# Performance work log

Measured on AMD Instinct MI355X. Metric: run time of the kernel, lower is better.

Reference implementation:

```python
import jax, jax.numpy as jnp
import numpy as np

EPS = 1e-5


def _conv3x3(x, w):
    # x: [B,C,H,W], w: [O,I,3,3], stride 1, padding 1
    return jax.lax.conv_general_dilated(
        x, w, window_strides=(1, 1), padding=((1, 1), (1, 1)),
        dimension_numbers=("NCHW", "OIHW", "NCHW"))


def _bn(x, g, b, m, v):
    # inference-mode BatchNorm2d over channel dim
    inv = jax.lax.rsqrt(v + EPS) * g
    return x * inv[None, :, None, None] + (b - m * inv)[None, :, None, None]


def setup_inputs() -> dict:
    key = jax.random.key(0)
    B, C, H, W = 32, 256, 56, 56
    ks = jax.random.split(key, 16)
    x = jax.random.normal(ks[0], (B, C, H, W), dtype=jnp.float32)
    mask = (jax.random.uniform(ks[1], (B, 1, H, W)) < 0.5).astype(jnp.float32)
    # dilated mask = 3x3 max-pool of mask
    mask_dilate = jax.lax.reduce_window(
        mask, -jnp.inf, jax.lax.max, (1, 1, 3, 3), (1, 1, 1, 1), "SAME")
    mask_dilate = jnp.maximum(mask_dilate, 0.0).astype(jnp.float32)
    vector = (jax.random.uniform(ks[2], (B, C)) < 0.5).astype(jnp.float32)
    conv1_w = jax.random.normal(ks[3], (C, C, 3, 3), dtype=jnp.float32) * 0.05
    conv2_w = jax.random.normal(ks[4], (C, C, 3, 3), dtype=jnp.float32) * 0.05
    bn1_g = 1.0 + 0.1 * jax.random.normal(ks[5], (C,), dtype=jnp.float32)
    bn1_b = 0.1 * jax.random.normal(ks[6], (C,), dtype=jnp.float32)
    bn1_m = 0.1 * jax.random.normal(ks[7], (C,), dtype=jnp.float32)
    bn1_v = 0.5 + jax.random.uniform(ks[8], (C,), dtype=jnp.float32)
    bn2_g = 1.0 + 0.1 * jax.random.normal(ks[9], (C,), dtype=jnp.float32)
    bn2_b = 0.1 * jax.random.normal(ks[10], (C,), dtype=jnp.float32)
    bn2_m = 0.1 * jax.random.normal(ks[11], (C,), dtype=jnp.float32)
    bn2_v = 0.5 + jax.random.uniform(ks[12], (C,), dtype=jnp.float32)
    return dict(x=x, mask=mask, mask_dilate=mask_dilate, vector=vector,
                conv1_w=conv1_w, bn1_g=bn1_g, bn1_b=bn1_b, bn1_m=bn1_m, bn1_v=bn1_v,
                conv2_w=conv2_w, bn2_g=bn2_g, bn2_b=bn2_b, bn2_m=bn2_m, bn2_v=bn2_v)


def reference(x, mask, mask_dilate, vector,
              conv1_w, bn1_g, bn1_b, bn1_m, bn1_v,
              conv2_w, bn2_g, bn2_b, bn2_m, bn2_v):
    # Sparse BasicBlock, stride=1, no downsample, input_mask=True.
    identity = x
    h = x * mask_dilate                      # apply_mask(x, mask_dilate)
    h = _conv3x3(h, conv1_w) * mask          # conv3x3_mask(conv1, ...)
    h = jax.nn.relu(_bn(h, bn1_g, bn1_b, bn1_m, bn1_v)) * mask_dilate  # bn_relu_mask(bn1, relu, ., mask_dilate)
    h = h * mask                             # apply_mask(x, mask)
    h = h * vector[:, :, None, None]         # channel_process(x, vector)
    h = _conv3x3(h, conv2_w) * mask          # conv3x3_mask(conv2, ...)
    h = _bn(h, bn2_g, bn2_b, bn2_m, bn2_v) * mask  # bn_relu_mask(bn2, None, ., mask)
    out = identity + h * mask                # identity + apply_mask(x, mask)
    return jax.nn.relu(out)
```

## Files before the change

kernel.cpp:

```cpp
#include <hip/hip_runtime.h>
#include <cstdint>


#define EPS 1e-5f

constexpr int Bn = 32, Cc = 256, Hh = 56, Ww = 56;
constexpr int HW = Hh * Ww;
constexpr int WP_ELEMS = 2 * 16 * 9 * 2 * 128 * 8;

typedef __bf16 bf16x8 __attribute__((ext_vector_type(8)));
typedef float  f32x16 __attribute__((ext_vector_type(16)));

__global__ void pack_xm(const float* __restrict__ x, const float* __restrict__ md,
                        __bf16* __restrict__ xm) {
    int blk = blockIdx.x, tid = threadIdx.x;
    int p = tid & 31, cg = tid >> 5;
    int px0 = blk * 32;
    int img = blk / 98;
    int s = (blk - img * 98) * 32 + p;
    float mdv = md[px0 + p];
    #pragma unroll
    for (int it = 0; it < 4; ++it) {
        int c = cg * 8 + it * 64;
        bf16x8 v;
        #pragma unroll
        for (int j = 0; j < 8; ++j)
            v[j] = (__bf16)(x[(size_t)(img * Cc + c + j) * HW + s] * mdv);
        *(bf16x8*)&xm[(size_t)(px0 + p) * Cc + c] = v;
    }
}

__global__ void pack_w(const float* __restrict__ w1, const float* __restrict__ w2,
                       __bf16* __restrict__ wp1, __bf16* __restrict__ wp2) {
    int id = blockIdx.x * 256 + threadIdx.x;
    const float* w = blockIdx.y ? w2 : w1;
    __bf16* wp = blockIdx.y ? wp2 : wp1;
    int j = id & 7; int t = id >> 3;
    int col = t & 127; t >>= 7;
    int half = t & 1; t >>= 1;
    int tap = t % 9; t /= 9;
    int chunk = t & 15; int coblk = t >> 4;
    int co = coblk * 128 + col;
    int ci = chunk * 16 + half * 8 + j;
    wp[id] = (__bf16)(w[((size_t)co * Cc + ci) * 9 + tap]);
}

__global__ void bn_prep(const float* g1, const float* b1, const float* m1, const float* v1,
                        const float* g2, const float* b2, const float* m2, const float* v2,
                        float* binv1, float* bbeta1, float* binv2, float* bbeta2) {
    int c = threadIdx.x;
    float i1 = g1[c] * rsqrtf(v1[c] + EPS);
    binv1[c] = i1; bbeta1[c] = b1[c] - m1[c] * i1;
    float i2 = g2[c] * rsqrtf(v2[c] + EPS);
    binv2[c] = i2; bbeta2[c] = b2[c] - m2[c] * i2;
}

__device__ __forceinline__ void gl_lds16(const __bf16* g, __bf16* l) {
    __builtin_amdgcn_global_load_lds(
        (const __attribute__((address_space(1))) void*)g,
        (__attribute__((address_space(3))) void*)l, 16, 0, 0);
}

template <bool C1>
__global__ __launch_bounds__(256, 2)
void conv_kern(const __bf16* __restrict__ src,
               const __bf16* __restrict__ wp,
               const float* __restrict__ maskg,
               const float* __restrict__ vec,
               const float* __restrict__ binv, const float* __restrict__ bbeta,
               const float* __restrict__ xin,
               void* __restrict__ dstv) {
    __shared__ __align__(16) __bf16 s_in[2 * 6 * 66 * 8];
    __shared__ __align__(16) __bf16 s_w[9 * 2 * 128 * 8];

    const int tid = threadIdx.x;
    const int lane = tid & 63, wave = tid >> 6;
    const int xlane = lane & 31, halfid = lane >> 5;
    const int band = blockIdx.x, coblk = blockIdx.y, img = blockIdx.z;
    const int y0 = band * 4;
    const int co0c = coblk * 128;
    const int pxw = C1 ? (wave >> 1) : (wave & 1);
    const int cow = C1 ? (wave & 1) : (wave >> 1);

    f32x16 acc[4][2];
    #pragma unroll
    for (int a = 0; a < 4; ++a)
        #pragma unroll
        for (int b = 0; b < 2; ++b)
            #pragma unroll
            for (int r = 0; r < 16; ++r) acc[a][b][r] = 0.f;

    const __bf16* wblk = wp + (size_t)coblk * (16 * 9 * 2 * 128 * 8);
    const float* maskp = maskg + (size_t)img * HW;

    for (int chunk = 0; chunk < 16; ++chunk) {
        __syncthreads();
        for (int e = tid; e < 792; e += 256) {
            int half = e & 1, r = e >> 1;
            int yy = r / 66, xx = r - yy * 66;
            int gy = y0 - 1 + yy, gx = xx - 1;
            bf16x8 v = {};
            if ((unsigned)gy < 56u && (unsigned)gx < 56u)
                v = *(const bf16x8*)&src[((size_t)(img * Hh + gy) * Ww + gx) * Cc +
                                          chunk * 16 + half * 8];
            *(bf16x8*)&s_in[((half * 6 + yy) * 66 + xx) * 8] = v;
        }
        {
            const __bf16* g = wblk + (size_t)chunk * (9 * 2 * 128 * 8);
            #pragma unroll
            for (int i = 0; i < 9; ++i) {
                int unit = wave * 576 + i * 64;
                gl_lds16(g + (size_t)(unit + lane) * 8, &s_w[unit * 8]);
            }
        }
        asm volatile("s_waitcnt vmcnt(0)" ::: "memory");
        __syncthreads();

        #pragma unroll
        for (int kh = 0; kh < 3; ++kh)
            #pragma unroll
            for (int kw = 0; kw < 3; ++kw) {
                const int tap = kh * 3 + kw;
                bf16x8 wf[2], inf[4];
                #pragma unroll
                for (int jt = 0; jt < 2; ++jt)
                    wf[jt] = *(const bf16x8*)&s_w[((tap * 2 + halfid) * 128 +
                                                   (cow * 2 + jt) * 32 + xlane) * 8];
                #pragma unroll
                for (int it = 0; it < 4; ++it) {
                    int tg = pxw * 4 + it;
                    int yy = (tg >> 1) + kh;
                    int xx = (tg & 1) * 32 + xlane + kw;
                    inf[it] = *(const bf16x8*)&s_in[((halfid * 6 + yy) * 66 + xx) * 8];
                }
                #pragma unroll
                for (int it = 0; it < 4; ++it)
                    #pragma unroll
                    for (int jt = 0; jt < 2; ++jt) {
                        if constexpr (C1)
                            acc[it][jt] = __builtin_amdgcn_mfma_f32_32x32x16_bf16(
                                inf[it], wf[jt], acc[it][jt], 0, 0, 0);
                        else
                            acc[it][jt] = __builtin_amdgcn_mfma_f32_32x32x16_bf16(
                                wf[jt], inf[it], acc[it][jt], 0, 0, 0);
                    }
            }
    }

    if constexpr (C1) {
        __bf16* u = (__bf16*)dstv;
        float iv[2], bt[2], vv[2]; int cog[2];
        #pragma unroll
        for (int jt = 0; jt < 2; ++jt) {
            cog[jt] = co0c + (cow * 2 + jt) * 32 + xlane;
            iv[jt] = binv[cog[jt]];
            bt[jt] = bbeta[cog[jt]];
            vv[jt] = vec[img * Cc + cog[jt]];
        }
        #pragma unroll
        for (int it = 0; it < 4; ++it) {
            int tg = pxw * 4 + it;
            int y = y0 + (tg >> 1), xb = (tg & 1) * 32;
            #pragma unroll
            for (int reg = 0; reg < 16; ++reg) {
                int x = xb + (reg & 3) + 8 * (reg >> 2) + 4 * halfid;
                if (x < 56) {
                    float mv = maskp[y * 56 + x];
                    size_t base = ((size_t)(img * Hh + y) * Ww + x) * Cc;
                    #pragma unroll
                    for (int jt = 0; jt < 2; ++jt) {
                        float o = fmaxf(fmaf(acc[it][jt][reg], iv[jt], bt[jt]), 0.f)
                                  * mv * vv[jt];
                        u[base + cog[jt]] = (__bf16)o;
                    }
                }
            }
        }
    } else {
        float* outp = (float*)dstv;
        int ya[4], xa[4]; float mva[4]; bool ok[4];
        #pragma unroll
        for (int it = 0; it < 4; ++it) {
            int tg = pxw * 4 + it;
            ya[it] = y0 + (tg >> 1);
            xa[it] = (tg & 1) * 32 + xlane;
            ok[it] = xa[it] < 56;
            mva[it] = ok[it] ? maskp[ya[it] * 56 + xa[it]] : 0.f;
        }
        #pragma unroll
        for (int jt = 0; jt < 2; ++jt) {
            int cb = co0c + (cow * 2 + jt) * 32;
            #pragma unroll
            for (int rg = 0; rg < 4; ++rg) {
                int c4 = cb + 8 * rg + 4 * halfid;
                float4 iv4 = *(const float4*)&binv[c4];
                float4 bt4 = *(const float4*)&bbeta[c4];
                float ivv[4] = {iv4.x, iv4.y, iv4.z, iv4.w};
                float btv[4] = {bt4.x, bt4.y, bt4.z, bt4.w};
                #pragma unroll
                for (int j = 0; j < 4; ++j) {
                    int reg = rg * 4 + j;
                    int co = c4 + j;
                    size_t cbase = (size_t)(img * Cc + co) * HW;
                    #pragma unroll
                    for (int it = 0; it < 4; ++it) {
                        if (ok[it]) {
                            size_t oa = cbase + ya[it] * 56 + xa[it];
                            float o = fmaxf(
                                xin[oa] + mva[it] * fmaf(acc[it][jt][reg], ivv[j], btv[j]),
                                0.f);
                            outp[oa] = o;
                        }
                    }
                }
            }
        }
    }
}

extern "C" void kernel_launch(void* const* d_in, const int* in_sizes, int n_in,
                              void* d_out, int out_size, void* d_ws, size_t ws_size,
                              hipStream_t stream) {
    const float* x    = (const float*)d_in[0];
    const float* mask = (const float*)d_in[1];
    const float* md   = (const float*)d_in[2];
    const float* vec  = (const float*)d_in[3];
    const float* w1   = (const float*)d_in[4];
    const float* bn1g = (const float*)d_in[5];
    const float* bn1b = (const float*)d_in[6];
    const float* bn1m = (const float*)d_in[7];
    const float* bn1v = (const float*)d_in[8];
    const float* w2   = (const float*)d_in[9];
    const float* bn2g = (const float*)d_in[10];
    const float* bn2b = (const float*)d_in[11];
    const float* bn2m = (const float*)d_in[12];
    const float* bn2v = (const float*)d_in[13];
    float* out = (float*)d_out;

    const size_t nhwc = (size_t)Bn * HW * Cc;
    __bf16* xm  = (__bf16*)d_ws;
    __bf16* u   = xm + nhwc;
    __bf16* wp1 = u + nhwc;
    __bf16* wp2 = wp1 + WP_ELEMS;
    float* binv1  = (float*)(wp2 + WP_ELEMS);
    float* bbeta1 = binv1 + 256;
    float* binv2  = bbeta1 + 256;
    float* bbeta2 = binv2 + 256;

    pack_xm<<<dim3(Bn * HW / 32), dim3(256), 0, stream>>>(x, md, xm);
    pack_w<<<dim3(WP_ELEMS / 256, 2), dim3(256), 0, stream>>>(w1, w2, wp1, wp2);
    bn_prep<<<dim3(1), dim3(256), 0, stream>>>(bn1g, bn1b, bn1m, bn1v,
                                               bn2g, bn2b, bn2m, bn2v,
                                               binv1, bbeta1, binv2, bbeta2);

    dim3 grid(14, 2, Bn);
    conv_kern<true><<<grid, dim3(256), 0, stream>>>(
        xm, wp1, mask, vec, binv1, bbeta1, nullptr, u);
    conv_kern<false><<<grid, dim3(256), 0, stream>>>(
        u, wp2, mask, nullptr, binv2, bbeta2, x, out);
}
```

Measured before the change: 536.0 us.

## Drop LDS staging; read pre-padded channel-blocked activations directly from global

Activations are repacked into a zero-padded [img][ci/8][58][66][8] bf16 layout so the conv kernels can read MFMA fragments straight from global memory with no bounds checks. This removes the shared-memory tiles, the per-chunk syncthreads and the LDS weight copies. The batch is processed in two groups of 16 images so the padded buffers stay small and cache-resident, and the intermediate buffer is zero-filled each group to keep its halo at zero. The cost is more launches, an extra zero-fill pass, and reliance on L1/L2 for reuse that LDS used to provide.

Measured after the change: 592.1 us. 10.5% more time.

```diff
diff --git a/kernel.cpp b/kernel.cpp
--- a/kernel.cpp
+++ b/kernel.cpp
@@ -4,30 +4,40 @@
 
 #define EPS 1e-5f
 
-constexpr int Bn = 32, Cc = 256, Hh = 56, Ww = 56;
-constexpr int HW = Hh * Ww;
-constexpr int WP_ELEMS = 2 * 16 * 9 * 2 * 128 * 8;
+constexpr int Cc = 256, Hh = 56, Ww = 56, HW = 3136;
+constexpr int NG = 16;
+constexpr int PH = 58, PW = 66;
+constexpr int PS = PH * PW * 8;
+constexpr int IPS = 32 * PS;
+constexpr int WP_EL = 16 * 9 * 2 * 256 * 8;
+constexpr int PACK_POS = NG * 32 * PH * PW;
 
 typedef __bf16 bf16x8 __attribute__((ext_vector_type(8)));
+typedef __bf16 bf16x4 __attribute__((ext_vector_type(4)));
 typedef float  f32x16 __attribute__((ext_vector_type(16)));
 
-__global__ void pack_xm(const float* __restrict__ x, const float* __restrict__ md,
-                        __bf16* __restrict__ xm) {
-    int blk = blockIdx.x, tid = threadIdx.x;
-    int p = tid & 31, cg = tid >> 5;
-    int px0 = blk * 32;
-    int img = blk / 98;
-    int s = (blk - img * 98) * 32 + p;
-    float mdv = md[px0 + p];
-    #pragma unroll
-    for (int it = 0; it < 4; ++it) {
-        int c = cg * 8 + it * 64;
-        bf16x8 v;
+__global__ void pack_xm2(const float* __restrict__ x, const float* __restrict__ md,
+                         __bf16* __restrict__ dst, int img0) {
+    int pos = blockIdx.x * 256 + threadIdx.x;
+    int xx = pos % PW; int t = pos / PW;
+    int yy = t % PH;  t /= PH;
+    int ci8 = t & 31; int il = t >> 5;
+    int img = img0 + il;
+    bf16x8 v = {};
+    int xi = xx - 1, yi = yy - 1;
+    if ((unsigned)xi < 56u && (unsigned)yi < 56u) {
+        float mdv = md[(size_t)img * HW + yi * 56 + xi];
         #pragma unroll
         for (int j = 0; j < 8; ++j)
-            v[j] = (__bf16)(x[(size_t)(img * Cc + c + j) * HW + s] * mdv);
-        *(bf16x8*)&xm[(size_t)(px0 + p) * Cc + c] = v;
-    }
+            v[j] = (__bf16)(x[((size_t)(img * Cc) + ci8 * 8 + j) * HW + yi * 56 + xi] * mdv);
+    }
+    *(bf16x8*)&dst[(size_t)pos * 8] = v;
+}
+
+__global__ void zero_fill(__bf16* __restrict__ dst) {
+    int pos = blockIdx.x * 256 + threadIdx.x;
+    bf16x8 z = {};
+    *(bf16x8*)&dst[(size_t)pos * 8] = z;
 }
 
 __global__ void pack_w(const float* __restrict__ w1, const float* __restrict__ w2,
@@ -36,11 +46,9 @@
     const float* w = blockIdx.y ? w2 : w1;
     __bf16* wp = blockIdx.y ? wp2 : wp1;
     int j = id & 7; int t = id >> 3;
-    int col = t & 127; t >>= 7;
+    int co = t & 255; t >>= 8;
     int half = t & 1; t >>= 1;
-    int tap = t % 9; t /= 9;
-    int chunk = t & 15; int coblk = t >> 4;
-    int co = coblk * 128 + col;
+    int tap = t % 9; int chunk = t / 9;
     int ci = chunk * 16 + half * 8 + j;
     wp[id] = (__bf16)(w[((size_t)co * Cc + ci) * 9 + tap]);
 }
@@ -55,166 +63,127 @@
     binv2[c] = i2; bbeta2[c] = b2[c] - m2[c] * i2;
 }
 
-__device__ __forceinline__ void gl_lds16(const __bf16* g, __bf16* l) {
-    __builtin_amdgcn_global_load_lds(
-        (const __attribute__((address_space(1))) void*)g,
-        (__attribute__((address_space(3))) void*)l, 16, 0, 0);
-}
-
 template <bool C1>
 __global__ __launch_bounds__(256, 2)
-void conv_kern(const __bf16* __restrict__ src,
+void conv_kern(const __bf16* __restrict__ pix,
                const __bf16* __restrict__ wp,
                const float* __restrict__ maskg,
                const float* __restrict__ vec,
                const float* __restrict__ binv, const float* __restrict__ bbeta,
                const float* __restrict__ xin,
-               void* __restrict__ dstv) {
-    __shared__ __align__(16) __bf16 s_in[2 * 6 * 66 * 8];
-    __shared__ __align__(16) __bf16 s_w[9 * 2 * 128 * 8];
-
+               void* __restrict__ dstv, int img0) {
     const int tid = threadIdx.x;
     const int lane = tid & 63, wave = tid >> 6;
     const int xlane = lane & 31, halfid = lane >> 5;
-    const int band = blockIdx.x, coblk = blockIdx.y, img = blockIdx.z;
-    const int y0 = band * 4;
-    const int co0c = coblk * 128;
-    const int pxw = C1 ? (wave >> 1) : (wave & 1);
-    const int cow = C1 ? (wave & 1) : (wave >> 1);
-
-    f32x16 acc[4][2];
+    const int band = blockIdx.x, cob = blockIdx.y, il = blockIdx.z;
+    const int img = img0 + il;
+    const int ybase = band * 4 + 2 * (wave >> 1);
+    const int c0 = cob * 128 + (wave & 1) * 64;
+
+    f32x16 acc[2][4];
     #pragma unroll
-    for (int a = 0; a < 4; ++a)
-        #pragma unroll
-        for (int b = 0; b < 2; ++b)
-            #pragma unroll
-            for (int r = 0; r < 16; ++r) acc[a][b][r] = 0.f;
-
-    const __bf16* wblk = wp + (size_t)coblk * (16 * 9 * 2 * 128 * 8);
-    const float* maskp = maskg + (size_t)img * HW;
+    for (int m = 0; m < 2; ++m)
+        #pragma unroll
+        for (int it = 0; it < 4; ++it)
+            #pragma unroll
+            for (int r = 0; r < 16; ++r) acc[m][it][r] = 0.f;
+
+    const __bf16* pimg = pix + (size_t)il * IPS;
 
     for (int chunk = 0; chunk < 16; ++chunk) {
-        __syncthreads();
-        for (int e = tid; e < 792; e += 256) {
-            int half = e & 1, r = e >> 1;
-            int yy = r / 66, xx = r - yy * 66;
-            int gy = y0 - 1 + yy, gx = xx - 1;
-            bf16x8 v = {};
-            if ((unsigned)gy < 56u && (unsigned)gx < 56u)
-                v = *(const bf16x8*)&src[((size_t)(img * Hh + gy) * Ww + gx) * Cc +
-                                          chunk * 16 + half * 8];
-            *(bf16x8*)&s_in[((half * 6 + yy) * 66 + xx) * 8] = v;
-        }
-        {
-            const __bf16* g = wblk + (size_t)chunk * (9 * 2 * 128 * 8);
-            #pragma unroll
-            for (int i = 0; i < 9; ++i) {
-                int unit = wave * 576 + i * 64;
-                gl_lds16(g + (size_t)(unit + lane) * 8, &s_w[unit * 8]);
+        const __bf16* wch = wp + (size_t)chunk * (9 * 2 * 256 * 8);
+        const __bf16* pch = pimg + (size_t)(chunk * 2 + halfid) * PS;
+        #pragma unroll
+        for (int kh = 0; kh < 3; ++kh) {
+            #pragma unroll
+            for (int kw = 0; kw < 3; ++kw) {
+                const int tap = kh * 3 + kw;
+                bf16x8 wf[2], pf[4];
+                #pragma unroll
+                for (int m = 0; m < 2; ++m)
+                    wf[m] = *(const bf16x8*)&wch[((size_t)(tap * 2 + halfid) * 256 +
+                                                  c0 + m * 32 + xlane) * 8];
+                #pragma unroll
+                for (int it = 0; it < 4; ++it) {
+                    int row = ybase + (it >> 1) + kh;
+                    int col = (it & 1) * 32 + kw + xlane;
+                    pf[it] = *(const bf16x8*)&pch[((size_t)row * PW + col) * 8];
+                }
+                #pragma unroll
+                for (int m = 0; m < 2; ++m)
+                    #pragma unroll
+                    for (int it = 0; it < 4; ++it)
+                        acc[m][it] = __builtin_amdgcn_mfma_f32_32x32x16_bf16(
+                            wf[m], pf[it], acc[m][it], 0, 0, 0);
             }
         }
-        asm volatile("s_waitcnt vmcnt(0)" ::: "memory");
-        __syncthreads();
-
-        #pragma unroll
-        for (int kh = 0; kh < 3; ++kh)
-            #pragma unroll
-            for (int kw = 0; kw < 3; ++kw) {
-                const int tap = kh * 3 + kw;
-                bf16x8 wf[2], inf[4];
-                #pragma unroll
-                for (int jt = 0; jt < 2; ++jt)
-                    wf[jt] = *(const bf16x8*)&s_w[((tap * 2 + halfid) * 128 +
-                                                   (cow * 2 + jt) * 32 + xlane) * 8];
+    }
+
+    float mv[4]; int yv[4], xv[4]; bool okv[4];
+    #pragma unroll
+    for (int it = 0; it < 4; ++it) {
+        yv[it] = ybase + (it >> 1);
+        xv[it] = (it & 1) * 32 + xlane;
+        okv[it] = xv[it] < 56;
+        mv[it] = okv[it] ? maskg[(size_t)img * HW + yv[it] * 56 + xv[it]] : 0.f;
+    }
+
+    if constexpr (C1) {
+        __bf16* u2 = (__bf16*)dstv;
+        #pragma unroll
+        for (int m = 0; m < 2; ++m)
+            #pragma unroll
+            for (int rg = 0; rg < 4; ++rg) {
+                const int c4 = c0 + m * 32 + rg * 8 + 4 * halfid;
+                const float4 iv4 = *(const float4*)&binv[c4];
+                const float4 bt4 = *(const float4*)&bbeta[c4];
+                const float4 vv4 = *(const float4*)&vec[img * Cc + c4];
+                const float ivv[4] = {iv4.x, iv4.y, iv4.z, iv4.w};
+                const float btv[4] = {bt4.x, bt4.y, bt4.z, bt4.w};
+                const float vvv[4] = {vv4.x, vv4.y, vv4.z, vv4.w};
+                const int co8 = (c0 + m * 32) / 8 + rg;
                 #pragma unroll
                 for (int it = 0; it < 4; ++it) {
-                    int tg = pxw * 4 + it;
-                    int yy = (tg >> 1) + kh;
-                    int xx = (tg & 1) * 32 + xlane + kw;
-                    inf[it] = *(const bf16x8*)&s_in[((halfid * 6 + yy) * 66 + xx) * 8];
-                }
-                #pragma unroll
-                for (int it = 0; it < 4; ++it)
-                    #pragma unroll
-                    for (int jt = 0; jt < 2; ++jt) {
-                        if constexpr (C1)
-                            acc[it][jt] = __builtin_amdgcn_mfma_f32_32x32x16_bf16(
-                                inf[it], wf[jt], acc[it][jt], 0, 0, 0);
-                        else
-                            acc[it][jt] = __builtin_amdgcn_mfma_f32_32x32x16_bf16(
-                                wf[jt], inf[it], acc[it][jt], 0, 0, 0);
-                    }
-            }
-    }
-
-    if constexpr (C1) {
-        __bf16* u = (__bf16*)dstv;
-        float iv[2], bt[2], vv[2]; int cog[2];
-        #pragma unroll
-        for (int jt = 0; jt < 2; ++jt) {
-            cog[jt] = co0c + (cow * 2 + jt) * 32 + xlane;
-            iv[jt] = binv[cog[jt]];
-            bt[jt] = bbeta[cog[jt]];
-            vv[jt] = vec[img * Cc + cog[jt]];
-        }
-        #pragma unroll
-        for (int it = 0; it < 4; ++it) {
-            int tg = pxw * 4 + it;
-            int y = y0 + (tg >> 1), xb = (tg & 1) * 32;
-            #pragma unroll
-            for (int reg = 0; reg < 16; ++reg) {
-                int x = xb + (reg & 3) + 8 * (reg >> 2) + 4 * halfid;
-                if (x < 56) {
-                    float mv = maskp[y * 56 + x];
-                    size_t base = ((size_t)(img * Hh + y) * Ww + x) * Cc;
-                    #pragma unroll
-                    for (int jt = 0; jt < 2; ++jt) {
-                        float o = fmaxf(fmaf(acc[it][jt][reg], iv[jt], bt[jt]), 0.f)
-                                  * mv * vv[jt];
-                        u[base + cog[jt]] = (__bf16)o;
+                    if (okv[it]) {
+                        bf16x4 h;
+                        #pragma unroll
+                        for (int j = 0; j < 4; ++j) {
+                            float o = fmaxf(fmaf(acc[m][it][rg * 4 + j], ivv[j], btv[j]), 0.f)
+                                      * mv[it] * vvv[j];
+                            h[j] = (__bf16)o;
+                        }
+                        size_t a = (((size_t)(il * 32 + co8) * PH + (yv[it] + 1)) * PW +
+                                    (xv[it] + 1)) * 8 + 4 * halfid;
+                        *(bf16x4*)&u2[a] = h;
                     }
                 }
             }
-        }
     } else {
         float* outp = (float*)dstv;
-        int ya[4], xa[4]; float mva[4]; bool ok[4];
-        #pragma unroll
-        for (int it = 0; it < 4; ++it) {
-            int tg = pxw * 4 + it;
-            ya[it] = y0 + (tg >> 1);
-            xa[it] = (tg & 1) * 32 + xlane;
-            ok[it] = xa[it] < 56;
-            mva[it] = ok[it] ? maskp[ya[it] * 56 + xa[it]] : 0.f;
-        }
-        #pragma unroll
-        for (int jt = 0; jt < 2; ++jt) {
-            int cb = co0c + (cow * 2 + jt) * 32;
+        #pragma unroll
+        for (int m = 0; m < 2; ++m)
             #pragma unroll
             for (int rg = 0; rg < 4; ++rg) {
-                int c4 = cb + 8 * rg + 4 * halfid;
-                float4 iv4 = *(const float4*)&binv[c4];
-                float4 bt4 = *(const float4*)&bbeta[c4];
-                float ivv[4] = {iv4.x, iv4.y, iv4.z, iv4.w};
-                float btv[4] = {bt4.x, bt4.y, bt4.z, bt4.w};
+                const int c4 = c0 + m * 32 + rg * 8 + 4 * halfid;
+                const float4 iv4 = *(const float4*)&binv[c4];
+                const float4 bt4 = *(const float4*)&bbeta[c4];
+                const float ivv[4] = {iv4.x, iv4.y, iv4.z, iv4.w};
+                const float btv[4] = {bt4.x, bt4.y, bt4.z, bt4.w};
                 #pragma unroll
                 for (int j = 0; j < 4; ++j) {
-                    int reg = rg * 4 + j;
-                    int co = c4 + j;
-                    size_t cbase = (size_t)(img * Cc + co) * HW;
+                    const size_t cbase = (size_t)(img * Cc + c4 + j) * HW;
                     #pragma unroll
                     for (int it = 0; it < 4; ++it) {
-                        if (ok[it]) {
-                            size_t oa = cbase + ya[it] * 56 + xa[it];
+                        if (okv[it]) {
+                            size_t oa = cbase + yv[it] * 56 + xv[it];
                             float o = fmaxf(
-                                xin[oa] + mva[it] * fmaf(acc[it][jt][reg], ivv[j], btv[j]),
+                                xin[oa] + mv[it] * fmaf(acc[m][it][rg * 4 + j], ivv[j], btv[j]),
                                 0.f);
                             outp[oa] = o;
                         }
                     }
                 }
             }
-        }
     }
 }
 
@@ -237,25 +206,28 @@
     const float* bn2v = (const float*)d_in[13];
     float* out = (float*)d_out;
 
-    const size_t nhwc = (size_t)Bn * HW * Cc;
-    __bf16* xm  = (__bf16*)d_ws;
-    __bf16* u   = xm + nhwc;
-    __bf16* wp1 = u + nhwc;
-    __bf16* wp2 = wp1 + WP_ELEMS;
-    float* binv1  = (float*)(wp2 + WP_ELEMS);
+    __bf16* xm2 = (__bf16*)d_ws;
+    __bf16* u2  = xm2 + (size_t)NG * IPS;
+    __bf16* wp1 = u2 + (size_t)NG * IPS;
+    __bf16* wp2 = wp1 + WP_EL;
+    float* binv1  = (float*)(wp2 + WP_EL);
     float* bbeta1 = binv1 + 256;
     float* binv2  = bbeta1 + 256;
     float* bbeta2 = binv2 + 256;
 
-    pack_xm<<<dim3(Bn * HW / 32), dim3(256), 0, stream>>>(x, md, xm);
-    pack_w<<<dim3(WP_ELEMS / 256, 2), dim3(256), 0, stream>>>(w1, w2, wp1, wp2);
+    pack_w<<<dim3(WP_EL / 256, 2), dim3(256), 0, stream>>>(w1, w2, wp1, wp2);
     bn_prep<<<dim3(1), dim3(256), 0, stream>>>(bn1g, bn1b, bn1m, bn1v,
                                                bn2g, bn2b, bn2m, bn2v,
                                                binv1, bbeta1, binv2, bbeta2);
 
-    dim3 grid(14, 2, Bn);
-    conv_kern<true><<<grid, dim3(256), 0, stream>>>(
-        xm, wp1, mask, vec, binv1, bbeta1, nullptr, u);
-    conv_kern<false><<<grid, dim3(256), 0, stream>>>(
-        u, wp2, mask, nullptr, binv2, bbeta2, x, out);
-}
+    for (int g = 0; g < 2; ++g) {
+        const int img0 = g * NG;
+        pack_xm2<<<dim3(PACK_POS / 256), dim3(256), 0, stream>>>(x, md, xm2, img0);
+        zero_fill<<<dim3(PACK_POS / 256), dim3(256), 0, stream>>>(u2);
+        dim3 grid(14, 2, NG);
+        conv_kern<true><<<grid, dim3(256), 0, stream>>>(
+            xm2, wp1, mask, vec, binv1, bbeta1, nullptr, u2, img0);
+        conv_kern<false><<<grid, dim3(256), 0, stream>>>(
+            u2, wp2, mask, nullptr, binv2, bbeta2, x, out, img0);
+    }
+}
```
